# Optimization experiments

Measured on AMD Instinct MI355X. Metric: run time of the kernel, lower is better.

## Reference

```python
import jax, jax.numpy as jnp
import numpy as np

N_NODES = 100000
N_EDGES = 3200000
C_FEAT = 512
F_OUT = 1


def setup_inputs() -> dict:
    key = jax.random.key(0)
    k1, k2, k3 = jax.random.split(key, 3)
    x = jax.random.normal(k1, (N_NODES, C_FEAT), dtype=jnp.float32)
    edge_index = jax.random.randint(k2, (2, N_EDGES), 0, N_NODES, dtype=jnp.int64)
    # GCNConv lin weight (glorot-ish scale) and zero-init bias, as in PyG defaults
    W = jax.random.normal(k3, (F_OUT, C_FEAT), dtype=jnp.float32) / np.sqrt(C_FEAT)
    b = jnp.zeros((F_OUT,), dtype=jnp.float32)
    return {"x": x, "edge_index": edge_index, "W": W, "b": b}


def reference(x, edge_index, W, b):
    N = x.shape[0]
    # GCNConv: project first (lin has no bias), then normalized aggregation
    h = x @ W.T  # [N, F_OUT]
    # add self-loops
    loops = jnp.arange(N, dtype=edge_index.dtype)
    row = jnp.concatenate([edge_index[0], loops])  # source
    col = jnp.concatenate([edge_index[1], loops])  # target
    # symmetric normalization: deg over targets (incl. self-loop weight 1)
    deg = jax.ops.segment_sum(jnp.ones_like(col, dtype=h.dtype), col, num_segments=N)
    dinv = jnp.where(deg > 0, jax.lax.rsqrt(deg), 0.0)
    norm = dinv[row] * dinv[col]  # [E+N]
    msg = h[row] * norm[:, None]  # gather + scale
    out = jax.ops.segment_sum(msg, col, num_segments=N) + b  # scatter-add + bias
    # F_out == 1 branch of forward
    return jax.nn.sigmoid(out)
```

## Files before the change

kernel.cpp:

```cpp
#include <hip/hip_runtime.h>
#include <hip/hip_fp16.h>
#include <math.h>

#define NN 100000
#define NE 3200000
#define CF 512

#define NPARTS  8
#define PART    12500
#define NSLICES 64
#define EPB     (NE / NSLICES)
#define NPB     (NSLICES * NPARTS)

#define OFF_G    12800000
#define OFF_DINV 13200000
#define OFF_FLAG 13600000

__global__ void detect_i64_kernel(const unsigned int* e32, int* flag) {
    unsigned v = e32[2 * threadIdx.x + 1];
    unsigned long long m = __ballot(v != 0u);
    if (threadIdx.x == 0) *flag = (m == 0ULL) ? 1 : 0;
}

__device__ __forceinline__ int4 load_col4(const int* __restrict__ e32, bool f64, int e) {
    if (f64) {
        const int4* q = (const int4*)(e32 + 2 * (NE + e));
        int4 a = q[0], b = q[1];
        return make_int4(a.x, a.z, b.x, b.z);
    }
    return *(const int4*)(e32 + NE + e);
}
__device__ __forceinline__ int load_row(const int* __restrict__ e32, bool f64, int e) {
    return f64 ? e32[2 * e] : e32[e];
}

__global__ __launch_bounds__(1024) void deg_lds_kernel(const int* __restrict__ e32,
                                                       const int* __restrict__ flag,
                                                       unsigned short* __restrict__ deg_part) {
    __shared__ int h[PART];
    int tid = threadIdx.x;
    for (int i = tid; i < PART; i += 1024) h[i] = 0;
    __syncthreads();
    int p = blockIdx.x >> 6;
    int s = blockIdx.x & 63;
    int lo = p * PART;
    bool f64 = (*flag) != 0;
    int base = s * EPB;
    for (int e = base + tid * 4; e < base + EPB; e += 4096) {
        int4 c = load_col4(e32, f64, e);
        unsigned l0 = (unsigned)(c.x - lo), l1 = (unsigned)(c.y - lo);
        unsigned l2 = (unsigned)(c.z - lo), l3 = (unsigned)(c.w - lo);
        if (l0 < PART) atomicAdd(&h[l0], 1);
        if (l1 < PART) atomicAdd(&h[l1], 1);
        if (l2 < PART) atomicAdd(&h[l2], 1);
        if (l3 < PART) atomicAdd(&h[l3], 1);
    }
    __syncthreads();
    unsigned short* out = deg_part + (size_t)blockIdx.x * PART;
    for (int i = tid; i < PART; i += 1024) out[i] = (unsigned short)h[i];
}

__global__ void dinv_kernel(const unsigned short* __restrict__ deg_part,
                            float* __restrict__ dinv) {
    int i = blockIdx.x * blockDim.x + threadIdx.x;
    if (i >= NN) return;
    int p = i / PART, l = i - p * PART;
    const unsigned short* bp = deg_part + ((size_t)(p << 6)) * PART + l;
    int d = 1;
#pragma unroll
    for (int s = 0; s < NSLICES; ++s) d += bp[(size_t)s * PART];
    dinv[i] = rsqrtf((float)d);
}

__global__ __launch_bounds__(256) void node_kernel(const float* __restrict__ x,
                                                   const float* __restrict__ W,
                                                   const float* __restrict__ dinv,
                                                   float* __restrict__ g) {
    int wave = (int)((blockIdx.x * blockDim.x + threadIdx.x) >> 6);
    int lane = threadIdx.x & 63;
    if (wave >= NN) return;
    const float4* xr = (const float4*)(x + (size_t)wave * CF);
    const float4* Wr = (const float4*)W;
    float sum = 0.f;
#pragma unroll
    for (int j = 0; j < 2; ++j) {
        float4 a = xr[lane + 64 * j];
        float4 w = Wr[lane + 64 * j];
        sum += a.x * w.x + a.y * w.y + a.z * w.z + a.w * w.w;
    }
#pragma unroll
    for (int off = 32; off >= 1; off >>= 1)
        sum += __shfl_down(sum, off, 64);
    if (lane == 0) g[wave] = sum * dinv[wave];
}

__global__ __launch_bounds__(1024) void scatter_lds_kernel(const int* __restrict__ e32,
                                                           const int* __restrict__ flag,
                                                           const float* __restrict__ g,
                                                           __half* __restrict__ s_part) {
    __shared__ float h[PART];
    int tid = threadIdx.x;
    for (int i = tid; i < PART; i += 1024) h[i] = 0.f;
    __syncthreads();
    int p = blockIdx.x >> 6;
    int s = blockIdx.x & 63;
    int lo = p * PART;
    bool f64 = (*flag) != 0;
    int base = s * EPB;
    for (int e = base + tid * 4; e < base + EPB; e += 4096) {
        int4 c = load_col4(e32, f64, e);
        unsigned l0 = (unsigned)(c.x - lo), l1 = (unsigned)(c.y - lo);
        unsigned l2 = (unsigned)(c.z - lo), l3 = (unsigned)(c.w - lo);
        if (l0 < PART) atomicAdd(&h[l0], g[load_row(e32, f64, e + 0)]);
        if (l1 < PART) atomicAdd(&h[l1], g[load_row(e32, f64, e + 1)]);
        if (l2 < PART) atomicAdd(&h[l2], g[load_row(e32, f64, e + 2)]);
        if (l3 < PART) atomicAdd(&h[l3], g[load_row(e32, f64, e + 3)]);
    }
    __syncthreads();
    __half* out = s_part + (size_t)blockIdx.x * PART;
    for (int i = tid; i < PART; i += 1024) out[i] = __float2half(h[i]);
}

__global__ void final_kernel(const __half* __restrict__ s_part,
                             const float* __restrict__ g,
                             const float* __restrict__ dinv,
                             const float* __restrict__ b,
                             float* __restrict__ out) {
    int i = blockIdx.x * blockDim.x + threadIdx.x;
    if (i >= NN) return;
    int p = i / PART, l = i - p * PART;
    const __half* bp = s_part + ((size_t)(p << 6)) * PART + l;
    float acc = g[i];
#pragma unroll
    for (int s = 0; s < NSLICES; ++s) acc += __half2float(bp[(size_t)s * PART]);
    float v = dinv[i] * acc + b[0];
    out[i] = 1.f / (1.f + expf(-v));
}

extern "C" void kernel_launch(void* const* d_in, const int* in_sizes, int n_in,
                              void* d_out, int out_size, void* d_ws, size_t ws_size,
                              hipStream_t stream) {
    const float* x = (const float*)d_in[0];
    const int* eidx = (const int*)d_in[1];
    const float* W = (const float*)d_in[2];
    const float* b = (const float*)d_in[3];
    float* out = (float*)d_out;

    char* ws = (char*)d_ws;
    unsigned short* part_u16 = (unsigned short*)(ws);
    __half* part_h = (__half*)(ws);
    float* g = (float*)(ws + OFF_G);
    float* dinv = (float*)(ws + OFF_DINV);
    int* flag = (int*)(ws + OFF_FLAG);

    detect_i64_kernel<<<1, 64, 0, stream>>>((const unsigned int*)eidx, flag);
    deg_lds_kernel<<<NPB, 1024, 0, stream>>>(eidx, flag, part_u16);
    dinv_kernel<<<(NN + 255) / 256, 256, 0, stream>>>(part_u16, dinv);
    node_kernel<<<(NN * 64 + 255) / 256, 256, 0, stream>>>(x, W, dinv, g);
    scatter_lds_kernel<<<NPB, 1024, 0, stream>>>(eidx, flag, g, part_h);
    final_kernel<<<(NN + 255) / 256, 256, 0, stream>>>(part_h, g, dinv, b, out);
}
```

Before: 364.4 us.

## Fuse node projection into degree histogram kernel and inline index-width detection

Splits each degree-histogram block so 12 waves build the LDS histogram while 4 waves compute the x·W projection for a slice of nodes. The latency-bound edge pass and the bandwidth-bound 200MB feature read then overlap, and the separate node kernel goes away. Dinv scaling of h moves into the dinv kernel. The int64 detection kernel is replaced by an in-kernel ballot, and the scatter kernel now loads row indices as int4 vectors. The trade-off is fewer waves per block for the histogram, which may slow that part.

Result: no change. 368.4 us (+1.1%).

```diff
diff --git a/kernel.cpp b/kernel.cpp
--- a/kernel.cpp
+++ b/kernel.cpp
@@ -12,14 +12,13 @@
 #define EPB     (NE / NSLICES)
 #define NPB     (NSLICES * NPARTS)
 
-#define OFF_G    12800000
-#define OFF_DINV 13200000
-#define OFF_FLAG 13600000
+#define OFF_H    12800000
+#define OFF_G    13200000
+#define OFF_DINV 13600000
 
-__global__ void detect_i64_kernel(const unsigned int* e32, int* flag) {
-    unsigned v = e32[2 * threadIdx.x + 1];
-    unsigned long long m = __ballot(v != 0u);
-    if (threadIdx.x == 0) *flag = (m == 0ULL) ? 1 : 0;
+__device__ __forceinline__ bool detect_f64(const int* __restrict__ e32) {
+    unsigned v = ((const unsigned*)e32)[2 * (threadIdx.x & 63) + 1];
+    return __ballot(v != 0u) == 0ULL;
 }
 
 __device__ __forceinline__ int4 load_col4(const int* __restrict__ e32, bool f64, int e) {
@@ -30,38 +29,84 @@
     }
     return *(const int4*)(e32 + NE + e);
 }
-__device__ __forceinline__ int load_row(const int* __restrict__ e32, bool f64, int e) {
-    return f64 ? e32[2 * e] : e32[e];
+
+__device__ __forceinline__ int4 load_row4(const int* __restrict__ e32, bool f64, int e) {
+    if (f64) {
+        const int4* q = (const int4*)(e32 + 2 * e);
+        int4 a = q[0], b = q[1];
+        return make_int4(a.x, a.z, b.x, b.z);
+    }
+    return *(const int4*)(e32 + e);
 }
 
-__global__ __launch_bounds__(1024) void deg_lds_kernel(const int* __restrict__ e32,
-                                                       const int* __restrict__ flag,
-                                                       unsigned short* __restrict__ deg_part) {
-    __shared__ int h[PART];
+#define NODES_PER_BLK 196
+
+__global__ __launch_bounds__(1024) void deg_h_kernel(const int* __restrict__ e32,
+                                                     const float* __restrict__ x,
+                                                     const float* __restrict__ W,
+                                                     unsigned short* __restrict__ deg_part,
+                                                     float* __restrict__ h) {
+    __shared__ int hist[PART];
     int tid = threadIdx.x;
-    for (int i = tid; i < PART; i += 1024) h[i] = 0;
+    for (int i = tid; i < PART; i += 1024) hist[i] = 0;
     __syncthreads();
-    int p = blockIdx.x >> 6;
-    int s = blockIdx.x & 63;
-    int lo = p * PART;
-    bool f64 = (*flag) != 0;
-    int base = s * EPB;
-    for (int e = base + tid * 4; e < base + EPB; e += 4096) {
-        int4 c = load_col4(e32, f64, e);
-        unsigned l0 = (unsigned)(c.x - lo), l1 = (unsigned)(c.y - lo);
-        unsigned l2 = (unsigned)(c.z - lo), l3 = (unsigned)(c.w - lo);
-        if (l0 < PART) atomicAdd(&h[l0], 1);
-        if (l1 < PART) atomicAdd(&h[l1], 1);
-        if (l2 < PART) atomicAdd(&h[l2], 1);
-        if (l3 < PART) atomicAdd(&h[l3], 1);
+
+    int w = tid >> 6, lane = tid & 63;
+    if (w < 12) {
+        bool f64 = detect_f64(e32);
+        int p = blockIdx.x >> 6;
+        int s = blockIdx.x & 63;
+        int lo = p * PART;
+        int base = s * EPB;
+        for (int e = base + tid * 4; e < base + EPB; e += 3072) {
+            int4 c = load_col4(e32, f64, e);
+            unsigned l0 = (unsigned)(c.x - lo), l1 = (unsigned)(c.y - lo);
+            unsigned l2 = (unsigned)(c.z - lo), l3 = (unsigned)(c.w - lo);
+            if (l0 < PART) atomicAdd(&hist[l0], 1);
+            if (l1 < PART) atomicAdd(&hist[l1], 1);
+            if (l2 < PART) atomicAdd(&hist[l2], 1);
+            if (l3 < PART) atomicAdd(&hist[l3], 1);
+        }
+    } else {
+        const float4* Wr = (const float4*)W;
+        float4 w0 = Wr[lane], w1 = Wr[lane + 64];
+        int start = blockIdx.x * NODES_PER_BLK;
+        int end = start + NODES_PER_BLK;
+        for (int i = start + (w - 12) * 2; i < end; i += 8) {
+            int i1 = i + 1;
+            float s0 = 0.f, s1 = 0.f;
+            if (i < NN) {
+                const float4* xr = (const float4*)(x + (size_t)i * CF);
+                float4 a = xr[lane], bq = xr[lane + 64];
+                s0 = a.x * w0.x + a.y * w0.y + a.z * w0.z + a.w * w0.w
+                   + bq.x * w1.x + bq.y * w1.y + bq.z * w1.z + bq.w * w1.w;
+            }
+            if (i1 < NN) {
+                const float4* xr = (const float4*)(x + (size_t)i1 * CF);
+                float4 a = xr[lane], bq = xr[lane + 64];
+                s1 = a.x * w0.x + a.y * w0.y + a.z * w0.z + a.w * w0.w
+                   + bq.x * w1.x + bq.y * w1.y + bq.z * w1.z + bq.w * w1.w;
+            }
+#pragma unroll
+            for (int off = 32; off >= 1; off >>= 1) {
+                s0 += __shfl_down(s0, off, 64);
+                s1 += __shfl_down(s1, off, 64);
+            }
+            if (lane == 0) {
+                if (i < NN) h[i] = s0;
+                if (i1 < NN) h[i1] = s1;
+            }
+        }
     }
     __syncthreads();
-    unsigned short* out = deg_part + (size_t)blockIdx.x * PART;
-    for (int i = tid; i < PART; i += 1024) out[i] = (unsigned short)h[i];
+    unsigned short* outp = deg_part + (size_t)blockIdx.x * PART;
+    for (int i = tid; i < PART; i += 1024) outp[i] = (unsigned short)hist[i];
 }
 
-__global__ void dinv_kernel(const unsigned short* __restrict__ deg_part,
-                            float* __restrict__ dinv) {
+__global__ void dinv_g_kernel(const unsigned short* __restrict__ deg_part,
+                              const float* __restrict__ h,
+                              float* __restrict__ dinv,
+                              float* __restrict__ g) {
     int i = blockIdx.x * blockDim.x + threadIdx.x;
     if (i >= NN) return;
     int p = i / PART, l = i - p * PART;
@@ -69,56 +114,37 @@
     int d = 1;
 #pragma unroll
     for (int s = 0; s < NSLICES; ++s) d += bp[(size_t)s * PART];
-    dinv[i] = rsqrtf((float)d);
-}
-
-__global__ __launch_bounds__(256) void node_kernel(const float* __restrict__ x,
-                                                   const float* __restrict__ W,
-                                                   const float* __restrict__ dinv,
-                                                   float* __restrict__ g) {
-    int wave = (int)((blockIdx.x * blockDim.x + threadIdx.x) >> 6);
-    int lane = threadIdx.x & 63;
-    if (wave >= NN) return;
-    const float4* xr = (const float4*)(x + (size_t)wave * CF);
-    const float4* Wr = (const float4*)W;
-    float sum = 0.f;
-#pragma unroll
-    for (int j = 0; j < 2; ++j) {
-        float4 a = xr[lane + 64 * j];
-        float4 w = Wr[lane + 64 * j];
-        sum += a.x * w.x + a.y * w.y + a.z * w.z + a.w * w.w;
-    }
-#pragma unroll
-    for (int off = 32; off >= 1; off >>= 1)
-        sum += __shfl_down(sum, off, 64);
-    if (lane == 0) g[wave] = sum * dinv[wave];
+    float di = rsqrtf((float)d);
+    dinv[i] = di;
+    g[i] = h[i] * di;
 }
 
 __global__ __launch_bounds__(1024) void scatter_lds_kernel(const int* __restrict__ e32,
-                                                           const int* __restrict__ flag,
                                                            const float* __restrict__ g,
                                                            __half* __restrict__ s_part) {
-    __shared__ float h[PART];
+    __shared__ float hs[PART];
     int tid = threadIdx.x;
-    for (int i = tid; i < PART; i += 1024) h[i] = 0.f;
+    for (int i = tid; i < PART; i += 1024) hs[i] = 0.f;
     __syncthreads();
+
+    bool f64 = detect_f64(e32);
     int p = blockIdx.x >> 6;
     int s = blockIdx.x & 63;
     int lo = p * PART;
-    bool f64 = (*flag) != 0;
     int base = s * EPB;
     for (int e = base + tid * 4; e < base + EPB; e += 4096) {
         int4 c = load_col4(e32, f64, e);
+        int4 r = load_row4(e32, f64, e);
         unsigned l0 = (unsigned)(c.x - lo), l1 = (unsigned)(c.y - lo);
         unsigned l2 = (unsigned)(c.z - lo), l3 = (unsigned)(c.w - lo);
-        if (l0 < PART) atomicAdd(&h[l0], g[load_row(e32, f64, e + 0)]);
-        if (l1 < PART) atomicAdd(&h[l1], g[load_row(e32, f64, e + 1)]);
-        if (l2 < PART) atomicAdd(&h[l2], g[load_row(e32, f64, e + 2)]);
-        if (l3 < PART) atomicAdd(&h[l3], g[load_row(e32, f64, e + 3)]);
+        if (l0 < PART) atomicAdd(&hs[l0], g[r.x]);
+        if (l1 < PART) atomicAdd(&hs[l1], g[r.y]);
+        if (l2 < PART) atomicAdd(&hs[l2], g[r.z]);
+        if (l3 < PART) atomicAdd(&hs[l3], g[r.w]);
     }
     __syncthreads();
-    __half* out = s_part + (size_t)blockIdx.x * PART;
-    for (int i = tid; i < PART; i += 1024) out[i] = __float2half(h[i]);
+    __half* outp = s_part + (size_t)blockIdx.x * PART;
+    for (int i = tid; i < PART; i += 1024) outp[i] = __float2half(hs[i]);
 }
 
 __global__ void final_kernel(const __half* __restrict__ s_part,
@@ -149,14 +175,12 @@
     char* ws = (char*)d_ws;
     unsigned short* part_u16 = (unsigned short*)(ws);
     __half* part_h = (__half*)(ws);
+    float* h = (float*)(ws + OFF_H);
     float* g = (float*)(ws + OFF_G);
     float* dinv = (float*)(ws + OFF_DINV);
-    int* flag = (int*)(ws + OFF_FLAG);
 
-    detect_i64_kernel<<<1, 64, 0, stream>>>((const unsigned int*)eidx, flag);
-    deg_lds_kernel<<<NPB, 1024, 0, stream>>>(eidx, flag, part_u16);
-    dinv_kernel<<<(NN + 255) / 256, 256, 0, stream>>>(part_u16, dinv);
-    node_kernel<<<(NN * 64 + 255) / 256, 256, 0, stream>>>(x, W, dinv, g);
-    scatter_lds_kernel<<<NPB, 1024, 0, stream>>>(eidx, flag, g, part_h);
+    deg_h_kernel<<<NPB, 1024, 0, stream>>>(eidx, x, W, part_u16, h);
+    dinv_g_kernel<<<(NN + 255) / 256, 256, 0, stream>>>(part_u16, h, dinv, g);
+    scatter_lds_kernel<<<NPB, 1024, 0, stream>>>(eidx, g, part_h);
     final_kernel<<<(NN + 255) / 256, 256, 0, stream>>>(part_h, g, dinv, b, out);
 }
```
